# Kernel tuning notes

Hardware: AMD Instinct MI355X
Metric: run time of the kernel (lower is better)

## Reference

```python
import jax, jax.numpy as jnp
import numpy as np

MAX_POINTS = 32
EPS = 1e-5


def setup_inputs() -> dict:
    key = jax.random.key(0)
    k1, k2, k3, k4, k5, k6 = jax.random.split(key, 6)
    M, P, C_IN, C_OUT = 40000, MAX_POINTS, 4, 64
    voxel_features = jax.random.normal(k1, (M, P, C_IN), dtype=jnp.float32)
    voxel_num_points = jax.random.randint(k2, (M,), 0, MAX_POINTS, dtype=jnp.int32)
    # Linear(C_in, C_out) params (PyTorch default init scale ~ U(-1/sqrt(fan_in), ...))
    lim = 1.0 / np.sqrt(C_IN)
    W = jax.random.uniform(k3, (C_OUT, C_IN), minval=-lim, maxval=lim, dtype=jnp.float32)
    b = jax.random.uniform(k4, (C_OUT,), minval=-lim, maxval=lim, dtype=jnp.float32)
    # BatchNorm1d affine params
    gamma = jnp.ones((C_OUT,), dtype=jnp.float32)
    beta = jnp.zeros((C_OUT,), dtype=jnp.float32)
    return {"voxel_features": voxel_features, "voxel_num_points": voxel_num_points,
            "W": W, "b": b, "gamma": gamma, "beta": beta}


def _vfe(x, n, W, b, gamma, beta):
    # x: (M, P, C_in), n: (M,) valid point counts
    mask = (jnp.arange(MAX_POINTS)[None, :] < n[:, None])            # (M, P)
    maskf = mask.astype(x.dtype)[..., None]                          # (M, P, 1)
    h = jnp.einsum('mpc,oc->mpo', x, W) + b                          # (M, P, C_out)
    h = h * maskf                                                    # zero invalid slots
    # BatchNorm1d (training-mode batch stats) over valid points only
    n_valid = jnp.maximum(jnp.sum(maskf), 1.0)
    mu = jnp.sum(h, axis=(0, 1)) / n_valid                           # (C_out,)
    d = (h - mu) * maskf
    var = jnp.sum(d * d, axis=(0, 1)) / n_valid                      # biased var, as BN
    hn = d * jax.lax.rsqrt(var + EPS) * gamma + beta * maskf
    hn = jax.nn.relu(hn) * maskf
    # per-voxel mean over valid points; voxels with n==0 output zeros
    counts = jnp.maximum(n.astype(x.dtype), 1.0)[:, None]
    return jnp.sum(hn, axis=1) / counts                              # (M, C_out)


def reference(voxel_features, voxel_num_points, W, b, gamma, beta):
    return _vfe(voxel_features, voxel_num_points, W, b, gamma, beta)
```

## Files before the change

### kernel.cpp

```cpp
#include <hip/hip_runtime.h>

#define MAX_POINTS 32
#define C_OUT 64
#define EPS 1e-5f

#define NMOM 15

__global__ __launch_bounds__(256) void vfe_stats(
    const float* __restrict__ x, const int* __restrict__ vnp,
    float* __restrict__ ws, int M)
{
    const int tid    = blockIdx.x * 256 + threadIdx.x;
    const int stride = gridDim.x * 256;
    const int total  = M * MAX_POINTS;

    float a[NMOM];
    #pragma unroll
    for (int i = 0; i < NMOM; ++i) a[i] = 0.f;

    const float4* __restrict__ xq = (const float4*)x;
    for (int i = tid; i < total; i += stride) {
        const int m = i >> 5;
        const int p = i & 31;
        const int n = vnp[m];
        const bool valid = p < n;
        float4 q = make_float4(0.f, 0.f, 0.f, 0.f);
        if (valid) q = xq[i];
        a[0] += q.x; a[1] += q.y; a[2] += q.z; a[3] += q.w;
        a[4]  = fmaf(q.x, q.x, a[4]);
        a[5]  = fmaf(q.x, q.y, a[5]);
        a[6]  = fmaf(q.x, q.z, a[6]);
        a[7]  = fmaf(q.x, q.w, a[7]);
        a[8]  = fmaf(q.y, q.y, a[8]);
        a[9]  = fmaf(q.y, q.z, a[9]);
        a[10] = fmaf(q.y, q.w, a[10]);
        a[11] = fmaf(q.z, q.z, a[11]);
        a[12] = fmaf(q.z, q.w, a[12]);
        a[13] = fmaf(q.w, q.w, a[13]);
        a[14] += valid ? 1.f : 0.f;
    }

    #pragma unroll
    for (int i = 0; i < NMOM; ++i) {
        float v = a[i];
        #pragma unroll
        for (int off = 32; off > 0; off >>= 1)
            v += __shfl_down(v, off, 64);
        a[i] = v;
    }

    __shared__ float bl[4][NMOM];
    const int lane = threadIdx.x & 63;
    const int wid  = threadIdx.x >> 6;
    if (lane == 0) {
        #pragma unroll
        for (int i = 0; i < NMOM; ++i) bl[wid][i] = a[i];
    }
    __syncthreads();
    if (threadIdx.x < NMOM) {
        const int i = threadIdx.x;
        atomicAdd(&ws[i], bl[0][i] + bl[1][i] + bl[2][i] + bl[3][i]);
    }
}

__global__ __launch_bounds__(256) void vfe_out(
    const float* __restrict__ x, const int* __restrict__ vnp,
    const float* __restrict__ W, const float* __restrict__ b,
    const float* __restrict__ gamma, const float* __restrict__ beta,
    const float* __restrict__ ws, float* __restrict__ out, int M)
{
    __shared__ float4 sx[32 * MAX_POINTS];
    const int lane = threadIdx.x & 63;
    const int wid  = threadIdx.x >> 6;

    const float4 w4  = ((const float4*)W)[lane];
    const float bias = b[lane];
    const float cnt  = ws[14];
    const float nv   = fmaxf(cnt, 1.0f);
    const float wdots = w4.x*ws[0] + w4.y*ws[1] + w4.z*ws[2] + w4.w*ws[3];
    const float S    = wdots + cnt * bias;
    const float mu   = S / nv;
    const float q2 = ws[4]*w4.x*w4.x + ws[8]*w4.y*w4.y + ws[11]*w4.z*w4.z + ws[13]*w4.w*w4.w
                   + 2.f*(ws[5]*w4.x*w4.y + ws[6]*w4.x*w4.z + ws[7]*w4.x*w4.w
                        + ws[9]*w4.y*w4.z + ws[10]*w4.y*w4.w + ws[12]*w4.z*w4.w);
    const float SS  = q2 + 2.f*bias*wdots + cnt*bias*bias;
    const float var = fmaxf(SS / nv - mu * mu, 0.f);
    const float A   = gamma[lane] * rsqrtf(var + EPS);
    const float B   = fmaf(-mu, A, beta[lane]);

    const int m0 = blockIdx.x * 32;

    const float4* __restrict__ xq = (const float4*)x + (size_t)m0 * MAX_POINTS;
    const int limit = min(1024, (M - m0) * MAX_POINTS);
    for (int t = threadIdx.x; t < limit; t += 256) sx[t] = xq[t];
    __syncthreads();

    #pragma unroll
    for (int v = 0; v < 8; ++v) {
        const int mv = wid * 8 + v;
        const int m  = m0 + mv;
        if (m >= M) break;
        const int n = vnp[m];
        const float4* __restrict__ q = &sx[mv * MAX_POINTS];
        float acc = 0.f;
        #pragma unroll 4
        for (int p = 0; p < n; ++p) {
            const float4 pt = q[p];
            const float h = fmaf(pt.x, w4.x, fmaf(pt.y, w4.y,
                            fmaf(pt.z, w4.z, fmaf(pt.w, w4.w, bias))));
            acc += fmaxf(fmaf(h, A, B), 0.f);
        }
        out[(size_t)m * C_OUT + lane] = acc / fmaxf((float)n, 1.0f);
    }
}

extern "C" void kernel_launch(void* const* d_in, const int* in_sizes, int n_in,
                              void* d_out, int out_size, void* d_ws, size_t ws_size,
                              hipStream_t stream) {
    const float* x     = (const float*)d_in[0];
    const int*   vnp   = (const int*)  d_in[1];
    const float* W     = (const float*)d_in[2];
    const float* b     = (const float*)d_in[3];
    const float* gamma = (const float*)d_in[4];
    const float* beta  = (const float*)d_in[5];
    float* out = (float*)d_out;
    float* ws  = (float*)d_ws;
    const int M = in_sizes[1];

    hipMemsetAsync(d_ws, 0, NMOM * sizeof(float), stream);
    vfe_stats<<<256, 256, 0, stream>>>(x, vnp, ws, M);
    const int nblk = (M + 31) / 32;
    vfe_out<<<nblk, 256, 0, stream>>>(x, vnp, W, b, gamma, beta, ws, out, M);
}
```

Baseline: 106.0 us.

## Spread stats atomics over sets, widen stats grid, drop LDS staging in output

The stats kernel now loads every point unconditionally and masks it by multiplying, rather than branching around the load. It runs with 2048 blocks instead of 256 and spreads its atomics over 8 partial-sum sets to reduce contention. The output kernel no longer stages voxels in shared memory behind a barrier. Each wave reads its 8 voxels' points directly as wave-uniform scalar loads, after summing the 8 partial moment sets. This removes LDS traffic and the barrier, but also reads invalid point slots in the stats pass and adds redundant moment reads per thread.

```diff
diff --git a/kernel.cpp b/kernel.cpp
--- a/kernel.cpp
+++ b/kernel.cpp
@@ -5,6 +5,7 @@
 #define EPS 1e-5f
 
 #define NMOM 15
+#define NSET 8
 
 __global__ __launch_bounds__(256) void vfe_stats(
     const float* __restrict__ x, const int* __restrict__ vnp,
@@ -20,24 +21,22 @@
 
     const float4* __restrict__ xq = (const float4*)x;
     for (int i = tid; i < total; i += stride) {
-        const int m = i >> 5;
-        const int p = i & 31;
-        const int n = vnp[m];
-        const bool valid = p < n;
-        float4 q = make_float4(0.f, 0.f, 0.f, 0.f);
-        if (valid) q = xq[i];
-        a[0] += q.x; a[1] += q.y; a[2] += q.z; a[3] += q.w;
-        a[4]  = fmaf(q.x, q.x, a[4]);
-        a[5]  = fmaf(q.x, q.y, a[5]);
-        a[6]  = fmaf(q.x, q.z, a[6]);
-        a[7]  = fmaf(q.x, q.w, a[7]);
-        a[8]  = fmaf(q.y, q.y, a[8]);
-        a[9]  = fmaf(q.y, q.z, a[9]);
-        a[10] = fmaf(q.y, q.w, a[10]);
-        a[11] = fmaf(q.z, q.z, a[11]);
-        a[12] = fmaf(q.z, q.w, a[12]);
-        a[13] = fmaf(q.w, q.w, a[13]);
-        a[14] += valid ? 1.f : 0.f;
+        const float4 q0 = xq[i];
+        const int   n   = vnp[i >> 5];
+        const float mk  = ((i & 31) < n) ? 1.f : 0.f;
+        const float qx = q0.x * mk, qy = q0.y * mk, qz = q0.z * mk, qw = q0.w * mk;
+        a[0] += qx; a[1] += qy; a[2] += qz; a[3] += qw;
+        a[4]  = fmaf(qx, qx, a[4]);
+        a[5]  = fmaf(qx, qy, a[5]);
+        a[6]  = fmaf(qx, qz, a[6]);
+        a[7]  = fmaf(qx, qw, a[7]);
+        a[8]  = fmaf(qy, qy, a[8]);
+        a[9]  = fmaf(qy, qz, a[9]);
+        a[10] = fmaf(qy, qw, a[10]);
+        a[11] = fmaf(qz, qz, a[11]);
+        a[12] = fmaf(qz, qw, a[12]);
+        a[13] = fmaf(qw, qw, a[13]);
+        a[14] += mk;
     }
 
     #pragma unroll
@@ -59,7 +58,8 @@
     __syncthreads();
     if (threadIdx.x < NMOM) {
         const int i = threadIdx.x;
-        atomicAdd(&ws[i], bl[0][i] + bl[1][i] + bl[2][i] + bl[3][i]);
+        const int set = blockIdx.x & (NSET - 1);
+        atomicAdd(&ws[set * 16 + i], bl[0][i] + bl[1][i] + bl[2][i] + bl[3][i]);
     }
 }
 
@@ -69,48 +69,52 @@
     const float* __restrict__ gamma, const float* __restrict__ beta,
     const float* __restrict__ ws, float* __restrict__ out, int M)
 {
-    __shared__ float4 sx[32 * MAX_POINTS];
     const int lane = threadIdx.x & 63;
-    const int wid  = threadIdx.x >> 6;
+    const int wid  = __builtin_amdgcn_readfirstlane(threadIdx.x >> 6);
+    const int gw   = blockIdx.x * 4 + wid;
+
+    float mom[NMOM];
+    #pragma unroll
+    for (int i = 0; i < NMOM; ++i) {
+        float s = 0.f;
+        #pragma unroll
+        for (int j = 0; j < NSET; ++j) s += ws[j * 16 + i];
+        mom[i] = s;
+    }
 
     const float4 w4  = ((const float4*)W)[lane];
     const float bias = b[lane];
-    const float cnt  = ws[14];
+    const float cnt  = mom[14];
     const float nv   = fmaxf(cnt, 1.0f);
-    const float wdots = w4.x*ws[0] + w4.y*ws[1] + w4.z*ws[2] + w4.w*ws[3];
-    const float S    = wdots + cnt * bias;
-    const float mu   = S / nv;
-    const float q2 = ws[4]*w4.x*w4.x + ws[8]*w4.y*w4.y + ws[11]*w4.z*w4.z + ws[13]*w4.w*w4.w
-                   + 2.f*(ws[5]*w4.x*w4.y + ws[6]*w4.x*w4.z + ws[7]*w4.x*w4.w
-                        + ws[9]*w4.y*w4.z + ws[10]*w4.y*w4.w + ws[12]*w4.z*w4.w);
+    const float wdots = w4.x*mom[0] + w4.y*mom[1] + w4.z*mom[2] + w4.w*mom[3];
+    const float mu   = (wdots + cnt * bias) / nv;
+    const float q2 = mom[4]*w4.x*w4.x + mom[8]*w4.y*w4.y + mom[11]*w4.z*w4.z + mom[13]*w4.w*w4.w
+                   + 2.f*(mom[5]*w4.x*w4.y + mom[6]*w4.x*w4.z + mom[7]*w4.x*w4.w
+                        + mom[9]*w4.y*w4.z + mom[10]*w4.y*w4.w + mom[12]*w4.z*w4.w);
     const float SS  = q2 + 2.f*bias*wdots + cnt*bias*bias;
     const float var = fmaxf(SS / nv - mu * mu, 0.f);
     const float A   = gamma[lane] * rsqrtf(var + EPS);
     const float B   = fmaf(-mu, A, beta[lane]);
 
-    const int m0 = blockIdx.x * 32;
-
-    const float4* __restrict__ xq = (const float4*)x + (size_t)m0 * MAX_POINTS;
-    const int limit = min(1024, (M - m0) * MAX_POINTS);
-    for (int t = threadIdx.x; t < limit; t += 256) sx[t] = xq[t];
-    __syncthreads();
-
+    const int m_base = gw * 8;
     #pragma unroll
     for (int v = 0; v < 8; ++v) {
-        const int mv = wid * 8 + v;
-        const int m  = m0 + mv;
+        const int m = m_base + v;
         if (m >= M) break;
         const int n = vnp[m];
-        const float4* __restrict__ q = &sx[mv * MAX_POINTS];
+        const float* __restrict__ xr = x + (size_t)m * (MAX_POINTS * 4);
         float acc = 0.f;
-        #pragma unroll 4
         for (int p = 0; p < n; ++p) {
-            const float4 pt = q[p];
-            const float h = fmaf(pt.x, w4.x, fmaf(pt.y, w4.y,
-                            fmaf(pt.z, w4.z, fmaf(pt.w, w4.w, bias))));
+            const float px = xr[p*4+0];
+            const float py = xr[p*4+1];
+            const float pz = xr[p*4+2];
+            const float pw = xr[p*4+3];
+            const float h = fmaf(px, w4.x, fmaf(py, w4.y,
+                            fmaf(pz, w4.z, fmaf(pw, w4.w, bias))));
             acc += fmaxf(fmaf(h, A, B), 0.f);
         }
-        out[(size_t)m * C_OUT + lane] = acc / fmaxf((float)n, 1.0f);
+        const float rn = 1.0f / fmaxf((float)n, 1.0f);
+        out[(size_t)m * C_OUT + lane] = acc * rn;
     }
 }
 
@@ -127,8 +131,9 @@
     float* ws  = (float*)d_ws;
     const int M = in_sizes[1];
 
-    hipMemsetAsync(d_ws, 0, NMOM * sizeof(float), stream);
-    vfe_stats<<<256, 256, 0, stream>>>(x, vnp, ws, M);
-    const int nblk = (M + 31) / 32;
+    hipMemsetAsync(d_ws, 0, NSET * 16 * sizeof(float), stream);
+    vfe_stats<<<2048, 256, 0, stream>>>(x, vnp, ws, M);
+    const int nwaves = (M + 7) / 8;
+    const int nblk   = (nwaves + 3) / 4;
     vfe_out<<<nblk, 256, 0, stream>>>(x, vnp, W, b, gamma, beta, ws, out, M);
 }
```

New measurement: 117.9 us. 11.3% more time.
